# Kernel optimization log

Measured on AMD Instinct MI355X. Metric: run time of the kernel, lower is better.

The kernel has to match this reference:

```python
import jax, jax.numpy as jnp
import numpy as np

KSIZE = 7
SIGMA = 3.0
ALPHA = 0.1
POS_VAL_FOR_ALL_NEG = 5.0
NEG_VAL_FOR_ALL_POS = -5.0


def _gauss_kernel():
    x = jnp.arange(KSIZE, dtype=jnp.float32) - (KSIZE - 1) / 2.0
    pdf = jnp.exp(-0.5 * (x / SIGMA) ** 2)
    return pdf / pdf.sum()


def _gaussian_blur(img):
    # img: (B, C, H, W); separable 7x7 gaussian, reflect padding (torchvision behavior)
    B, C, H, W = img.shape
    k = _gauss_kernel()
    pad = KSIZE // 2
    x = jnp.pad(img, ((0, 0), (0, 0), (pad, pad), (pad, pad)), mode='reflect')
    x = x.reshape(B * C, 1, H + 2 * pad, W + 2 * pad)
    kh = k.reshape(1, 1, KSIZE, 1)
    kw = k.reshape(1, 1, 1, KSIZE)
    x = jax.lax.conv_general_dilated(x, kh, (1, 1), 'VALID')
    x = jax.lax.conv_general_dilated(x, kw, (1, 1), 'VALID')
    return x.reshape(B, C, H, W)


def _dup_map(x, mask, fallback):
    # x, mask: (L,). Gather x[mask] (original order) then tile to length L.
    # Stable argsort puts True(=selected) positions first in original order.
    L = x.shape[0]
    cnt = mask.sum()
    order = jnp.argsort(jnp.logical_not(mask))  # selected indices first, stable
    idx = order[jnp.arange(L) % jnp.maximum(cnt, 1)]
    return jnp.where(cnt == 0, jnp.float32(fallback), x[idx])


_dup_vmapped = jax.vmap(_dup_map, in_axes=(0, 0, None))


def _bce_with_logits(x, y):
    # mean( max(x,0) - x*y + log1p(exp(-|x|)) ) == mean( softplus(x) - x*y )
    return jnp.mean(jnp.logaddexp(0.0, x) - x * y)


def _forward(inp, tgt):
    B, C, H, W = inp.shape
    aug_sim_target = (_gaussian_blur(tgt * 255.0) > 0).astype(jnp.float32)

    L = H * W
    x = inp.reshape(B * C, L)
    t = tgt.reshape(B * C, L)
    a = aug_sim_target.reshape(B * C, L)

    # duplicated_pos: gather input at target>0, tile; fallback +5 if no positives
    pos_mask = t > 0
    dup_pos = _dup_vmapped(x, pos_mask, POS_VAL_FOR_ALL_NEG)

    # duplicated_false_pos: prefer (input>0 & ~aug_pos); else all negatives; else -5
    aug_pos = a > 0
    fp_mask = jnp.logical_and(x > 0, jnp.logical_not(aug_pos))
    neg_mask = jnp.logical_not(aug_pos)
    cnt_fp = fp_mask.sum(axis=1, keepdims=True)
    chosen_mask = jnp.where(cnt_fp > 0, fp_mask, neg_mask)
    dup_fp = _dup_vmapped(x, chosen_mask, NEG_VAL_FOR_ALL_POS)

    sim = dup_pos * x
    aug_sim = dup_pos * dup_fp

    sim_loss = _bce_with_logits(sim, t) + _bce_with_logits(dup_pos, jnp.ones_like(x))
    aug_sim_loss = _bce_with_logits(aug_sim, jnp.zeros_like(x))
    return sim_loss + ALPHA * aug_sim_loss


def setup_inputs() -> dict:
    key = jax.random.key(0)
    k1, k2 = jax.random.split(key)
    B, C, H, W = 16, 3, 512, 512
    inp = jax.random.normal(k1, (B, C, H, W), dtype=jnp.float32)
    tgt = jax.random.randint(k2, (B, C, H, W), 0, 2).astype(jnp.float32)
    return {"input": inp, "target": tgt}


def reference(input, target):
    return _forward(input, target)
```

## Files before the change

kernel.cpp:

```cpp
#include <hip/hip_runtime.h>
#include <math.h>

constexpr int W = 512;
constexpr int HIMG = 512;
constexpr int L = 1 << 18;
constexpr int LOG2L = 18;
constexpr int TPB = 256;
constexpr int TILE = 2048;
constexpr int TILES_PER_ROW = L / TILE;
constexpr int WORDS_PER_TILE = TILE / 64;
constexpr int SPB = 32;
constexpr int HALO = 3;
constexpr int HBUF = SPB + 2 * HALO;
constexpr int BLK_PER_IMG = HIMG / SPB;
constexpr int LBLK = 32;
constexpr int CHUNK = L / LBLK;
constexpr int LIT = CHUNK / (TPB * 4);

typedef unsigned long long ull;

__device__ __forceinline__ float softplus_f(float v) {
    return fmaxf(v, 0.0f) +
           0.6931471805599453f *
               __builtin_amdgcn_logf(1.0f + __builtin_amdgcn_exp2f(-fabsf(v) * 1.4426950408889634f));
}

__device__ __forceinline__ ull hdil7(ull prev, ull cur, ull next) {
    ull r = cur;
    r |= (cur >> 1) | (next << 63);
    r |= (cur >> 2) | (next << 62);
    r |= (cur >> 3) | (next << 61);
    r |= (cur << 1) | (prev >> 63);
    r |= (cur << 2) | (prev >> 62);
    r |= (cur << 3) | (prev >> 61);
    return r;
}

template <typename T>
__device__ __forceinline__ T sel8(const T* a, int k) {
    return k == 0 ? a[0] : k == 1 ? a[1] : k == 2 ? a[2] : k == 3 ? a[3]
         : k == 4 ? a[4] : k == 5 ? a[5] : k == 6 ? a[6] : a[7];
}

__global__ __launch_bounds__(TPB)
void fused_mask_kernel(const float* __restrict__ x, const float* __restrict__ t,
                       ull* __restrict__ mT, ull* __restrict__ mFp, ull* __restrict__ mNeg,
                       int* __restrict__ cPos, int* __restrict__ cFp, int* __restrict__ cNeg,
                       float* __restrict__ out) {
    if (blockIdx.x == 0 && threadIdx.x == 0) out[0] = 0.0f;
    int b = blockIdx.x;
    int img = b >> 4;
    int y0 = (b & 15) * SPB;
    int gs0 = img * HIMG + y0;

    __shared__ ull hbuf[HBUF][8];
    __shared__ ull tbuf[SPB][8];
    __shared__ ull xbuf[SPB][8];

    int lane = threadIdx.x & 63;
    int wv = threadIdx.x >> 6;
    int ylo = (y0 - HALO < 0) ? 0 : y0 - HALO;
    int yhi = (y0 + SPB - 1 + HALO > HIMG - 1) ? HIMG - 1 : y0 + SPB - 1 + HALO;

    for (int yl = ylo + wv; yl <= yhi; yl += 4) {
        int gbase = (img * HIMG + yl) * W;
        bool own = (yl >= y0) && (yl < y0 + SPB);
        ull wt[8], wx[8], h[8];
#pragma unroll
        for (int k = 0; k < 8; ++k) wt[k] = __ballot(t[gbase + k * 64 + lane] > 0.0f);
        if (own) {
#pragma unroll
            for (int k = 0; k < 8; ++k) wx[k] = __ballot(x[gbase + k * 64 + lane] > 0.0f);
        }
#pragma unroll
        for (int k = 0; k < 8; ++k) {
            ull cur = wt[k];
            ull prev = k ? wt[k - 1]
                         : ((((cur >> 1) & 1ull) << 63) | (((cur >> 2) & 1ull) << 62) |
                            (((cur >> 3) & 1ull) << 61));
            ull next = (k < 7) ? wt[k + 1]
                               : (((cur >> 62) & 1ull) | (((cur >> 61) & 1ull) << 1) |
                                  (((cur >> 60) & 1ull) << 2));
            h[k] = hdil7(prev, cur, next);
        }
        int hy = yl - (y0 - HALO);
        int k = lane & 7;
        if (lane < 8) {
            hbuf[hy][k] = sel8(h, k);
        } else if (own && lane < 16) {
            tbuf[yl - y0][k] = sel8(wt, k);
            mT[(img * HIMG + yl) * 8 + k] = sel8(wt, k);
        } else if (own && lane < 24) {
            xbuf[yl - y0][k] = sel8(wx, k);
        }
    }
    __syncthreads();

    int tid = threadIdx.x;
    int ys = tid >> 3;
    int c = tid & 7;
    int y = y0 + ys;
    ull wa = 0;
#pragma unroll
    for (int d = -3; d <= 3; ++d) {
        int yy = y + d;
        yy = yy < 0 ? -yy : (yy > HIMG - 1 ? 2 * (HIMG - 1) - yy : yy);
        wa |= hbuf[yy - (y0 - HALO)][c];
    }
    ull tw = tbuf[ys][c];
    ull fp = xbuf[ys][c] & ~wa;
    ull ng = ~wa;
    int gw = gs0 * 8 + tid;
    mFp[gw] = fp;
    mNeg[gw] = ng;
    int pT = __popcll(tw), pF = __popcll(fp), pN = __popcll(ng);
#pragma unroll
    for (int m = 1; m < 32; m <<= 1) {
        pT += __shfl_xor(pT, m, 64);
        pF += __shfl_xor(pF, m, 64);
        pN += __shfl_xor(pN, m, 64);
    }
    if ((lane & 31) == 0) {
        int tile = img * TILES_PER_ROW + (y0 >> 2) + (tid >> 5);
        cPos[tile] = pT; cFp[tile] = pF; cNeg[tile] = pN;
    }
}

__global__ void scan_kernel(const int* __restrict__ cPos, const int* __restrict__ cFp,
                            const int* __restrict__ cNeg,
                            int* __restrict__ oPos, int* __restrict__ oCh,
                            int* __restrict__ rCp, int* __restrict__ rCc,
                            ull* __restrict__ rMp, ull* __restrict__ rMc,
                            int* __restrict__ rUseFp) {
    int r = blockIdx.x;
    int tid = threadIdx.x;
    __shared__ int ssp[TILES_PER_ROW], ssf[TILES_PER_ROW], ssn[TILES_PER_ROW];
    int myp = cPos[r * TILES_PER_ROW + tid];
    int myf = cFp[r * TILES_PER_ROW + tid];
    int myn = cNeg[r * TILES_PER_ROW + tid];
    ssp[tid] = myp; ssf[tid] = myf; ssn[tid] = myn;
    __syncthreads();
    for (int off = 1; off < TILES_PER_ROW; off <<= 1) {
        int ap = 0, af = 0, an = 0;
        if (tid >= off) { ap = ssp[tid - off]; af = ssf[tid - off]; an = ssn[tid - off]; }
        __syncthreads();
        if (tid >= off) { ssp[tid] += ap; ssf[tid] += af; ssn[tid] += an; }
        __syncthreads();
    }
    int cp = ssp[TILES_PER_ROW - 1], cf = ssf[TILES_PER_ROW - 1], cn = ssn[TILES_PER_ROW - 1];
    bool useFp = cf > 0;
    int tile = r * TILES_PER_ROW + tid;
    oPos[tile] = ssp[tid] - myp;
    oCh[tile] = useFp ? (ssf[tid] - myf) : (ssn[tid] - myn);
    if (tid == 0) {
        int cc = useFp ? cf : cn;
        rCp[r] = cp; rCc[r] = cc; rUseFp[r] = useFp ? 1 : 0;
        ull dp_ = (ull)(cp > 0 ? cp : 1);
        ull dc_ = (ull)(cc > 0 ? cc : 1);
        rMp[r] = ((1ull << 40) + dp_ - 1) / dp_;
        rMc[r] = ((1ull << 40) + dc_ - 1) / dc_;
    }
}

__global__ __launch_bounds__(TPB)
void scatter_kernel(const float* __restrict__ x, const ull* __restrict__ mT,
                    const ull* __restrict__ mFp, const ull* __restrict__ mNeg,
                    const int* __restrict__ oPos, const int* __restrict__ oCh,
                    const int* __restrict__ rUseFp,
                    float* __restrict__ xp, float* __restrict__ xf) {
    int tile = blockIdx.x;
    int tid = threadIdx.x;
    int r = tile >> 7;
    bool useFp = rUseFp[r] != 0;
    int widx = tile * WORDS_PER_TILE + (tid >> 3);
    int shift = (tid & 7) * 8;
    unsigned bT = (unsigned)(mT[widx] >> shift) & 0xFF;
    ull chw = useFp ? mFp[widx] : mNeg[widx];
    unsigned bCh = (unsigned)(chw >> shift) & 0xFF;
    const float4* x4 = (const float4*)x;
    int b4 = tile * (TILE / 4) + tid * 2;
    float4 a = x4[b4], b = x4[b4 + 1];
    float xv[8] = {a.x, a.y, a.z, a.w, b.x, b.y, b.z, b.w};
    int p = __popc(bT), c = __popc(bCh);
    __shared__ int s[TPB];
    __shared__ float bufP[TILE], bufC[TILE];
    int v = p | (c << 16);
    s[tid] = v;
    __syncthreads();
    for (int off = 1; off < TPB; off <<= 1) {
        int add = tid >= off ? s[tid - off] : 0;
        __syncthreads();
        s[tid] += add;
        __syncthreads();
    }
    int excl = s[tid] - v;
    int ep = excl & 0xFFFF;
    int ec = excl >> 16;
#pragma unroll
    for (int e = 0; e < 8; ++e) {
        if ((bT >> e) & 1) bufP[ep++] = xv[e];
        if ((bCh >> e) & 1) bufC[ec++] = xv[e];
    }
    __syncthreads();
    int tot = s[TPB - 1];
    int P = tot & 0xFFFF, C = tot >> 16;
    int rL = r << LOG2L;
    int pbase = rL + oPos[tile];
    for (int i = tid; i < P; i += TPB) xp[pbase + i] = bufP[i];
    int cbase = rL + oCh[tile];
    for (int i = tid; i < C; i += TPB) xf[cbase + i] = bufC[i];
}

__global__ __launch_bounds__(TPB)
void loss_kernel(const float* __restrict__ x, const ull* __restrict__ mT,
                 const float* __restrict__ xp, const float* __restrict__ xf,
                 const int* __restrict__ rCp, const int* __restrict__ rCc,
                 const ull* __restrict__ rMp, const ull* __restrict__ rMc,
                 float* __restrict__ out, double inv_ntot) {
    int r = blockIdx.x >> 5;
    int cb = (blockIdx.x & 31) * CHUNK;
    int rL = r << LOG2L;
    int cp = rCp[r], cc = rCc[r];
    ull Mp = rMp[r], Mc = rMc[r];
    const float4* x4 = (const float4*)(x + rL + cb);
    const float* xpr = xp + rL;
    const float* xfr = xf + rL;
    const ull* mtr = mT + (rL >> 6);
    float local = 0.0f;
#pragma unroll
    for (int it = 0; it < LIT; ++it) {
        int o4 = it * TPB + threadIdx.x;
        unsigned l = (unsigned)(cb + (o4 << 2));
        float4 xv = x4[o4];
        unsigned tb = (unsigned)(mtr[l >> 6] >> (l & 63)) & 0xFu;
        float dps[4], dfs[4];
        if (cp > 0) {
            unsigned d = (unsigned)cp;
            unsigned q = (unsigned)(((ull)l * Mp) >> 40);
            unsigned m0 = l - q * d;
            unsigned m1 = m0 + 1; if (m1 == d) m1 = 0;
            unsigned m2 = m1 + 1; if (m2 == d) m2 = 0;
            unsigned m3 = m2 + 1; if (m3 == d) m3 = 0;
            dps[0] = xpr[m0]; dps[1] = xpr[m1]; dps[2] = xpr[m2]; dps[3] = xpr[m3];
        } else {
            dps[0] = dps[1] = dps[2] = dps[3] = 5.0f;
        }
        if (cc > 0) {
            unsigned d = (unsigned)cc;
            unsigned q = (unsigned)(((ull)l * Mc) >> 40);
            unsigned m0 = l - q * d;
            unsigned m1 = m0 + 1; if (m1 == d) m1 = 0;
            unsigned m2 = m1 + 1; if (m2 == d) m2 = 0;
            unsigned m3 = m2 + 1; if (m3 == d) m3 = 0;
            dfs[0] = xfr[m0]; dfs[1] = xfr[m1]; dfs[2] = xfr[m2]; dfs[3] = xfr[m3];
        } else {
            dfs[0] = dfs[1] = dfs[2] = dfs[3] = -5.0f;
        }
        float xs[4] = {xv.x, xv.y, xv.z, xv.w};
#pragma unroll
        for (int k = 0; k < 4; ++k) {
            float sim = dps[k] * xs[k];
            float e = softplus_f(sim) + softplus_f(-dps[k]) + 0.1f * softplus_f(dps[k] * dfs[k]);
            if ((tb >> k) & 1) e -= sim;
            local += e;
        }
    }
    __shared__ double sd[TPB];
    int tid = threadIdx.x;
    sd[tid] = (double)local;
    __syncthreads();
    for (int off = TPB / 2; off > 0; off >>= 1) {
        if (tid < off) sd[tid] += sd[tid + off];
        __syncthreads();
    }
    if (tid == 0) atomicAdd(out, (float)(sd[0] * inv_ntot));
}

extern "C" void kernel_launch(void* const* d_in, const int* in_sizes, int n_in,
                              void* d_out, int out_size, void* d_ws, size_t ws_size,
                              hipStream_t stream) {
    const float* x = (const float*)d_in[0];
    const float* t = (const float*)d_in[1];
    float* out = (float*)d_out;

    int ntot = in_sizes[0];
    int R = ntot >> LOG2L;
    int numTiles = ntot / TILE;
    int nwords = ntot / 64;
    int nMaskBlk = ntot / (SPB * W);

    char* ws = (char*)d_ws;
    size_t off = 0;
    auto alloc = [&](size_t bytes) {
        size_t p = off;
        off = (off + bytes + 255) & ~(size_t)255;
        return (void*)(ws + p);
    };
    ull* mT   = (ull*)alloc((size_t)nwords * 8);
    ull* mFp  = (ull*)alloc((size_t)nwords * 8);
    ull* mNeg = (ull*)alloc((size_t)nwords * 8);
    int* cPos = (int*)alloc(numTiles * sizeof(int));
    int* cFp  = (int*)alloc(numTiles * sizeof(int));
    int* cNeg = (int*)alloc(numTiles * sizeof(int));
    int* oPos = (int*)alloc(numTiles * sizeof(int));
    int* oCh  = (int*)alloc(numTiles * sizeof(int));
    int* rCp = (int*)alloc(R * sizeof(int));
    int* rCc = (int*)alloc(R * sizeof(int));
    int* rUseFp = (int*)alloc(R * sizeof(int));
    ull* rMp = (ull*)alloc(R * sizeof(ull));
    ull* rMc = (ull*)alloc(R * sizeof(ull));
    float* xp = (float*)alloc((size_t)ntot * sizeof(float));
    float* xf = (float*)alloc((size_t)ntot * sizeof(float));

    fused_mask_kernel<<<nMaskBlk, TPB, 0, stream>>>(x, t, mT, mFp, mNeg, cPos, cFp, cNeg, out);
    scan_kernel<<<R, TILES_PER_ROW, 0, stream>>>(cPos, cFp, cNeg, oPos, oCh,
                                                 rCp, rCc, rMp, rMc, rUseFp);
    scatter_kernel<<<numTiles, TPB, 0, stream>>>(x, mT, mFp, mNeg, oPos, oCh, rUseFp, xp, xf);
    loss_kernel<<<R * LBLK, TPB, 0, stream>>>(x, mT, xp, xf, rCp, rCc, rMp, rMc, out,
                                              1.0 / (double)ntot);
}
```

Before: 171.6 us.

## Remap loss blocks per XCD, batch gathers ahead of compute, use wave-shuffle reduction

The loss kernel now splits each row into 64 chunks and maps block IDs so that all blocks of a given row land on the same XCD. This is meant to keep each row's gathered xp/xf data in one L2. It also issues all loads and gathers for a thread's elements before any softplus math, to expose memory-level parallelism. The shared-memory tree reduction is replaced with a wave shuffle plus a 4-entry shared sum. The mapping hardcodes 48 rows and 8 XCDs (r = xcd*6 + ...), which is fragile for other shapes, and more values held in registers may lower occupancy.

Result: slower. 190.7 us (+11.1%).

```diff
diff --git a/kernel.cpp b/kernel.cpp
--- a/kernel.cpp
+++ b/kernel.cpp
@@ -12,10 +12,9 @@
 constexpr int SPB = 32;
 constexpr int HALO = 3;
 constexpr int HBUF = SPB + 2 * HALO;
-constexpr int BLK_PER_IMG = HIMG / SPB;
-constexpr int LBLK = 32;
+constexpr int LBLK = 64;
 constexpr int CHUNK = L / LBLK;
-constexpr int LIT = CHUNK / (TPB * 4);
+constexpr int G = CHUNK / (TPB * 4);
 
 typedef unsigned long long ull;
 
@@ -217,8 +216,12 @@
                  const int* __restrict__ rCp, const int* __restrict__ rCc,
                  const ull* __restrict__ rMp, const ull* __restrict__ rMc,
                  float* __restrict__ out, double inv_ntot) {
-    int r = blockIdx.x >> 5;
-    int cb = (blockIdx.x & 31) * CHUNK;
+    int b = blockIdx.x;
+    int xcd = b & 7;
+    int i = b >> 3;
+    int r = xcd * 6 + (i >> 6);
+    int chunk = i & 63;
+    int cb = chunk * CHUNK;
     int rL = r << LOG2L;
     int cp = rCp[r], cc = rCc[r];
     ull Mp = rMp[r], Mc = rMc[r];
@@ -226,54 +229,81 @@
     const float* xpr = xp + rL;
     const float* xfr = xf + rL;
     const ull* mtr = mT + (rL >> 6);
-    float local = 0.0f;
-#pragma unroll
-    for (int it = 0; it < LIT; ++it) {
-        int o4 = it * TPB + threadIdx.x;
-        unsigned l = (unsigned)(cb + (o4 << 2));
-        float4 xv = x4[o4];
-        unsigned tb = (unsigned)(mtr[l >> 6] >> (l & 63)) & 0xFu;
-        float dps[4], dfs[4];
-        if (cp > 0) {
-            unsigned d = (unsigned)cp;
+    int tid = threadIdx.x;
+
+    float4 xv[G];
+    ull tw[G];
+    unsigned l0[G];
+    float dps[G][4], dfs[G][4];
+#pragma unroll
+    for (int g = 0; g < G; ++g) {
+        int o4 = g * TPB + tid;
+        l0[g] = (unsigned)(cb + (o4 << 2));
+        xv[g] = x4[o4];
+        tw[g] = mtr[l0[g] >> 6];
+    }
+    if (cp > 0) {
+        unsigned d = (unsigned)cp;
+#pragma unroll
+        for (int g = 0; g < G; ++g) {
+            unsigned l = l0[g];
             unsigned q = (unsigned)(((ull)l * Mp) >> 40);
             unsigned m0 = l - q * d;
             unsigned m1 = m0 + 1; if (m1 == d) m1 = 0;
             unsigned m2 = m1 + 1; if (m2 == d) m2 = 0;
             unsigned m3 = m2 + 1; if (m3 == d) m3 = 0;
-            dps[0] = xpr[m0]; dps[1] = xpr[m1]; dps[2] = xpr[m2]; dps[3] = xpr[m3];
-        } else {
-            dps[0] = dps[1] = dps[2] = dps[3] = 5.0f;
-        }
-        if (cc > 0) {
-            unsigned d = (unsigned)cc;
+            dps[g][0] = xpr[m0]; dps[g][1] = xpr[m1];
+            dps[g][2] = xpr[m2]; dps[g][3] = xpr[m3];
+        }
+    } else {
+#pragma unroll
+        for (int g = 0; g < G; ++g)
+            dps[g][0] = dps[g][1] = dps[g][2] = dps[g][3] = 5.0f;
+    }
+    if (cc > 0) {
+        unsigned d = (unsigned)cc;
+#pragma unroll
+        for (int g = 0; g < G; ++g) {
+            unsigned l = l0[g];
             unsigned q = (unsigned)(((ull)l * Mc) >> 40);
             unsigned m0 = l - q * d;
             unsigned m1 = m0 + 1; if (m1 == d) m1 = 0;
             unsigned m2 = m1 + 1; if (m2 == d) m2 = 0;
             unsigned m3 = m2 + 1; if (m3 == d) m3 = 0;
-            dfs[0] = xfr[m0]; dfs[1] = xfr[m1]; dfs[2] = xfr[m2]; dfs[3] = xfr[m3];
-        } else {
-            dfs[0] = dfs[1] = dfs[2] = dfs[3] = -5.0f;
-        }
-        float xs[4] = {xv.x, xv.y, xv.z, xv.w};
+            dfs[g][0] = xfr[m0]; dfs[g][1] = xfr[m1];
+            dfs[g][2] = xfr[m2]; dfs[g][3] = xfr[m3];
+        }
+    } else {
+#pragma unroll
+        for (int g = 0; g < G; ++g)
+            dfs[g][0] = dfs[g][1] = dfs[g][2] = dfs[g][3] = -5.0f;
+    }
+
+    float local = 0.0f;
+#pragma unroll
+    for (int g = 0; g < G; ++g) {
+        unsigned tb = (unsigned)(tw[g] >> (l0[g] & 63)) & 0xFu;
+        float xs[4] = {xv[g].x, xv[g].y, xv[g].z, xv[g].w};
 #pragma unroll
         for (int k = 0; k < 4; ++k) {
-            float sim = dps[k] * xs[k];
-            float e = softplus_f(sim) + softplus_f(-dps[k]) + 0.1f * softplus_f(dps[k] * dfs[k]);
+            float dp = dps[g][k];
+            float sim = dp * xs[k];
+            float e = softplus_f(sim) + softplus_f(-dp) + 0.1f * softplus_f(dp * dfs[g][k]);
             if ((tb >> k) & 1) e -= sim;
             local += e;
         }
     }
-    __shared__ double sd[TPB];
-    int tid = threadIdx.x;
-    sd[tid] = (double)local;
-    __syncthreads();
-    for (int off = TPB / 2; off > 0; off >>= 1) {
-        if (tid < off) sd[tid] += sd[tid + off];
-        __syncthreads();
-    }
-    if (tid == 0) atomicAdd(out, (float)(sd[0] * inv_ntot));
+
+#pragma unroll
+    for (int m = 1; m < 64; m <<= 1) local += __shfl_xor(local, m, 64);
+    __shared__ double sw[4];
+    int lane = tid & 63, wv = tid >> 6;
+    if (lane == 0) sw[wv] = (double)local;
+    __syncthreads();
+    if (tid == 0) {
+        double s = sw[0] + sw[1] + sw[2] + sw[3];
+        atomicAdd(out, (float)(s * inv_ntot));
+    }
 }
 
 extern "C" void kernel_launch(void* const* d_in, const int* in_sizes, int n_in,
```

## Specialize loss kernel for fallback false-positive case by grouping tiled duplicates

Applied to the files above, without the earlier changes.

Adds a fast path for rows with no chosen false-positive elements and at least a third of elements positive. It iterates over each gathered positive value once and handles every output position that tiles onto it. The softplus terms that depend only on that value are computed once and scaled by the repeat count, which removes modulo indexing, gather loads and redundant transcendental calls. It also doubles the blocks per row and replaces the shared-memory tree reduction with wavefront shuffles. The added branch increases code size, and correctness depends on the launch grid matching the new 64-blocks-per-row mapping.

New measurement: 190.7 us. 1.11x slower.

```diff
diff --git a/kernel.cpp b/kernel.cpp
--- a/kernel.cpp
+++ b/kernel.cpp
@@ -12,10 +12,10 @@
 constexpr int SPB = 32;
 constexpr int HALO = 3;
 constexpr int HBUF = SPB + 2 * HALO;
-constexpr int BLK_PER_IMG = HIMG / SPB;
-constexpr int LBLK = 32;
+constexpr int LBLK = 64;
 constexpr int CHUNK = L / LBLK;
-constexpr int LIT = CHUNK / (TPB * 4);
+constexpr int G = CHUNK / (TPB * 4);
+constexpr int JPB = 8 * TPB;
 
 typedef unsigned long long ull;
 
@@ -217,63 +217,98 @@
                  const int* __restrict__ rCp, const int* __restrict__ rCc,
                  const ull* __restrict__ rMp, const ull* __restrict__ rMc,
                  float* __restrict__ out, double inv_ntot) {
-    int r = blockIdx.x >> 5;
-    int cb = (blockIdx.x & 31) * CHUNK;
+    int b = blockIdx.x;
+    int r = b >> 6;
+    int blk = b & 63;
     int rL = r << LOG2L;
     int cp = rCp[r], cc = rCc[r];
-    ull Mp = rMp[r], Mc = rMc[r];
-    const float4* x4 = (const float4*)(x + rL + cb);
+    const float* xr = x + rL;
     const float* xpr = xp + rL;
-    const float* xfr = xf + rL;
     const ull* mtr = mT + (rL >> 6);
+    int tid = threadIdx.x;
     float local = 0.0f;
-#pragma unroll
-    for (int it = 0; it < LIT; ++it) {
-        int o4 = it * TPB + threadIdx.x;
-        unsigned l = (unsigned)(cb + (o4 << 2));
-        float4 xv = x4[o4];
-        unsigned tb = (unsigned)(mtr[l >> 6] >> (l & 63)) & 0xFu;
-        float dps[4], dfs[4];
-        if (cp > 0) {
-            unsigned d = (unsigned)cp;
-            unsigned q = (unsigned)(((ull)l * Mp) >> 40);
-            unsigned m0 = l - q * d;
-            unsigned m1 = m0 + 1; if (m1 == d) m1 = 0;
-            unsigned m2 = m1 + 1; if (m2 == d) m2 = 0;
-            unsigned m3 = m2 + 1; if (m3 == d) m3 = 0;
-            dps[0] = xpr[m0]; dps[1] = xpr[m1]; dps[2] = xpr[m2]; dps[3] = xpr[m3];
-        } else {
-            dps[0] = dps[1] = dps[2] = dps[3] = 5.0f;
-        }
-        if (cc > 0) {
-            unsigned d = (unsigned)cc;
-            unsigned q = (unsigned)(((ull)l * Mc) >> 40);
-            unsigned m0 = l - q * d;
-            unsigned m1 = m0 + 1; if (m1 == d) m1 = 0;
-            unsigned m2 = m1 + 1; if (m2 == d) m2 = 0;
-            unsigned m3 = m2 + 1; if (m3 == d) m3 = 0;
-            dfs[0] = xfr[m0]; dfs[1] = xfr[m1]; dfs[2] = xfr[m2]; dfs[3] = xfr[m3];
-        } else {
-            dfs[0] = dfs[1] = dfs[2] = dfs[3] = -5.0f;
-        }
-        float xs[4] = {xv.x, xv.y, xv.z, xv.w};
-#pragma unroll
-        for (int k = 0; k < 4; ++k) {
-            float sim = dps[k] * xs[k];
-            float e = softplus_f(sim) + softplus_f(-dps[k]) + 0.1f * softplus_f(dps[k] * dfs[k]);
-            if ((tb >> k) & 1) e -= sim;
-            local += e;
-        }
-    }
-    __shared__ double sd[TPB];
-    int tid = threadIdx.x;
-    sd[tid] = (double)local;
-    __syncthreads();
-    for (int off = TPB / 2; off > 0; off >>= 1) {
-        if (tid < off) sd[tid] += sd[tid + off];
-        __syncthreads();
-    }
-    if (tid == 0) atomicAdd(out, (float)(sd[0] * inv_ntot));
+
+    if (cc == 0 && cp * 3 >= L) {
+        for (int base = blk * JPB; base < cp; base += 64 * JPB) {
+#pragma unroll
+            for (int it = 0; it < 8; ++it) {
+                int j = base + it * TPB + tid;
+                if (j < cp) {
+                    float dp = xpr[j];
+                    int l2 = j + cp, l3 = l2 + cp;
+                    bool b2 = l2 < L, b3 = l3 < L;
+                    float x1 = xr[j];
+                    float x2 = b2 ? xr[l2] : 0.0f;
+                    float x3 = b3 ? xr[l3] : 0.0f;
+                    unsigned t1 = (unsigned)(mtr[j >> 6] >> (j & 63)) & 1u;
+                    unsigned t2 = b2 ? ((unsigned)(mtr[l2 >> 6] >> (l2 & 63)) & 1u) : 0u;
+                    unsigned t3 = b3 ? ((unsigned)(mtr[l3 >> 6] >> (l3 & 63)) & 1u) : 0u;
+                    float n = 1.0f + (b2 ? 1.0f : 0.0f) + (b3 ? 1.0f : 0.0f);
+                    float sim1 = dp * x1, sim2 = dp * x2, sim3 = dp * x3;
+                    float e = softplus_f(sim1) - (t1 ? sim1 : 0.0f);
+                    e += b2 ? (softplus_f(sim2) - (t2 ? sim2 : 0.0f)) : 0.0f;
+                    e += b3 ? (softplus_f(sim3) - (t3 ? sim3 : 0.0f)) : 0.0f;
+                    e += n * (softplus_f(-dp) + 0.1f * softplus_f(-5.0f * dp));
+                    local += e;
+                }
+            }
+        }
+    } else {
+        int cb = blk * CHUNK;
+        ull Mp = rMp[r], Mc = rMc[r];
+        const float* xfr = xf + rL;
+        const float4* x4 = (const float4*)(xr + cb);
+#pragma unroll
+        for (int g = 0; g < G; ++g) {
+            int o4 = g * TPB + tid;
+            unsigned l = (unsigned)(cb + (o4 << 2));
+            float4 xv = x4[o4];
+            unsigned tb = (unsigned)(mtr[l >> 6] >> (l & 63)) & 0xFu;
+            float dps[4], dfs[4];
+            if (cp > 0) {
+                unsigned d = (unsigned)cp;
+                unsigned q = (unsigned)(((ull)l * Mp) >> 40);
+                unsigned m0 = l - q * d;
+                unsigned m1 = m0 + 1; if (m1 == d) m1 = 0;
+                unsigned m2 = m1 + 1; if (m2 == d) m2 = 0;
+                unsigned m3 = m2 + 1; if (m3 == d) m3 = 0;
+                dps[0] = xpr[m0]; dps[1] = xpr[m1]; dps[2] = xpr[m2]; dps[3] = xpr[m3];
+            } else {
+                dps[0] = dps[1] = dps[2] = dps[3] = 5.0f;
+            }
+            if (cc > 0) {
+                unsigned d = (unsigned)cc;
+                unsigned q = (unsigned)(((ull)l * Mc) >> 40);
+                unsigned m0 = l - q * d;
+                unsigned m1 = m0 + 1; if (m1 == d) m1 = 0;
+                unsigned m2 = m1 + 1; if (m2 == d) m2 = 0;
+                unsigned m3 = m2 + 1; if (m3 == d) m3 = 0;
+                dfs[0] = xfr[m0]; dfs[1] = xfr[m1]; dfs[2] = xfr[m2]; dfs[3] = xfr[m3];
+            } else {
+                dfs[0] = dfs[1] = dfs[2] = dfs[3] = -5.0f;
+            }
+            float xs[4] = {xv.x, xv.y, xv.z, xv.w};
+#pragma unroll
+            for (int k = 0; k < 4; ++k) {
+                float dp = dps[k];
+                float sim = dp * xs[k];
+                float e = softplus_f(sim) + softplus_f(-dp) + 0.1f * softplus_f(dp * dfs[k]);
+                if ((tb >> k) & 1) e -= sim;
+                local += e;
+            }
+        }
+    }
+
+#pragma unroll
+    for (int m = 1; m < 64; m <<= 1) local += __shfl_xor(local, m, 64);
+    __shared__ double sw[4];
+    int lane = tid & 63, wv = tid >> 6;
+    if (lane == 0) sw[wv] = (double)local;
+    __syncthreads();
+    if (tid == 0) {
+        double s = sw[0] + sw[1] + sw[2] + sw[3];
+        atomicAdd(out, (float)(s * inv_ntot));
+    }
 }
 
 extern "C" void kernel_launch(void* const* d_in, const int* in_sizes, int n_in,
```
